# Kernel optimization log

Hardware: AMD Instinct MI355X
Metric: run time of the kernel (lower is better)

Reference implementation:

```python
import jax, jax.numpy as jnp
import numpy as np

B, T, P, N, U, L, K = 32, 12, 12, 512, 64, 2, 2
C = 2 * U  # combined_dim = input_dim(rnn_units) + rnn_units = 128


def setup_inputs():
    ks = jax.random.split(jax.random.key(0), 24)
    inp = {
        'x': jax.random.normal(ks[0], (B, T, N, 1), jnp.float32),
        'adj': jax.random.uniform(ks[1], (N, N), jnp.float32),
        'spatial_mask_1': 0.1 * jax.random.normal(ks[2], (N, N), jnp.float32),
        'spatial_mask_2': 0.1 * jax.random.normal(ks[3], (N, N), jnp.float32),
        'temporal_mask': 0.1 * jax.random.normal(ks[4], (T, N), jnp.float32),
        'fc_in_w': 0.1 * jax.random.normal(ks[5], (1, U), jnp.float32),
        'fc_in_b': jnp.zeros((U,), jnp.float32),
        'fc_out_w': 0.1 * jax.random.normal(ks[6], (U, 1), jnp.float32),
        'fc_out_b': jnp.zeros((1,), jnp.float32),
    }
    i = 7
    for pre in ('enc', 'dec'):
        for name, od in (('w_ru', 2 * U), ('w_c', U), ('w_ru2', 2 * U), ('w_c2', U)):
            inp[pre + '_' + name] = 0.08 * jax.random.normal(ks[i], (L, 2 * K, C, od), jnp.float32)
            i += 1
            inp[pre + '_' + name.replace('w', 'b')] = jnp.zeros((L, od), jnp.float32)
    return inp


def _supports(adj):
    # adj_hat = A + I; fwd = D_out^-1 A_hat ; bwd = D_in^-1 A_hat^T (inf -> 0)
    ah = adj + jnp.eye(adj.shape[0], dtype=adj.dtype)
    d_out = ah.sum(1)
    d_in = ah.sum(0)
    inv_out = jnp.where(d_out > 0, 1.0 / d_out, 0.0)
    inv_in = jnp.where(d_in > 0, 1.0 / d_in, 0.0)
    return inv_out[:, None] * ah, inv_in[:, None] * ah.T


def _dgc(x, sup, w, b):
    # x: [B,N,C]; sup: (fwd,bwd) each [N,N]; w: [2K,C,O]; b: [O]
    # The torch code expands x K times per support, so each k-slice of x_out is
    # identical: sum_k P_s @ w[k] == P_s @ w[sK:(s+1)K].sum(0). Same math, fused.
    pf = jnp.einsum('nm,bni->bmi', sup[0], x)
    pb = jnp.einsum('nm,bni->bmi', sup[1], x)
    return (jnp.einsum('bni,io->bno', pf, w[:K].sum(0))
            + jnp.einsum('bni,io->bno', pb, w[K:].sum(0)) + b)


def _cell(x, h, s1, s2, w_ru, b_ru, w_c, b_c, w_ru2, b_ru2, w_c2, b_c2):
    xh = jnp.concatenate([x, h], axis=-1)
    r1, u1 = jnp.split(jax.nn.sigmoid(_dgc(xh, s1, w_ru, b_ru)), 2, axis=-1)
    c1 = jnp.tanh(_dgc(jnp.concatenate([x, r1 * h], axis=-1), s1, w_c, b_c))
    r2, u2 = jnp.split(jax.nn.sigmoid(_dgc(xh, s2, w_ru2, b_ru2)), 2, axis=-1)
    c2 = jnp.tanh(_dgc(jnp.concatenate([x, r2 * h], axis=-1), s2, w_c2, b_c2))
    u = 0.5 * (u1 + u2)
    c = 0.5 * (c1 + c2)
    return (1.0 - u) * h + u * c


def _forward(x, adj, sm1, sm2, tm, fc_in_w, fc_in_b, fc_out_w, fc_out_b, enc, dec):
    x = x * (jnp.tanh(tm) + 1.0)[None, :, :, None]
    adj1 = adj * (jnp.tanh(0.5 * (sm1 + sm1.T)) + 1.0)
    adj2 = adj * (jnp.tanh(0.5 * (sm2 + sm2.T)) + 1.0)
    s1 = _supports(adj1)
    s2 = _supports(adj2)

    def run_layers(cells, inp, h):
        hs = []
        for i in range(L):
            hi = _cell(inp, h[i], s1, s2, *[p[i] for p in cells])
            hs.append(hi)
            inp = hi
        return jnp.stack(hs)

    def enc_step(h, xt):
        inp = xt @ fc_in_w + fc_in_b  # [B,N,U]
        return run_layers(enc, inp, h), None

    h0 = jnp.zeros((L, B, N, U), x.dtype)
    h, _ = jax.lax.scan(enc_step, h0, jnp.swapaxes(x, 0, 1))

    def dec_step(carry, _):
        h, go = carry
        inp = go @ fc_in_w + fc_in_b
        h = run_layers(dec, inp, h)
        out_t = h[-1] @ fc_out_w + fc_out_b  # [B,N,1]
        return (h, out_t), out_t

    _, outs = jax.lax.scan(dec_step, (h, jnp.zeros((B, N, 1), x.dtype)), None, length=P)
    return jnp.swapaxes(outs, 0, 1)[..., 0]  # [B,P,N]


def reference(x, adj, spatial_mask_1, spatial_mask_2, temporal_mask,
              fc_in_w, fc_in_b, fc_out_w, fc_out_b,
              enc_w_ru, enc_b_ru, enc_w_c, enc_b_c, enc_w_ru2, enc_b_ru2, enc_w_c2, enc_b_c2,
              dec_w_ru, dec_b_ru, dec_w_c, dec_b_c, dec_w_ru2, dec_b_ru2, dec_w_c2, dec_b_c2):
    enc = (enc_w_ru, enc_b_ru, enc_w_c, enc_b_c, enc_w_ru2, enc_b_ru2, enc_w_c2, enc_b_c2)
    dec = (dec_w_ru, dec_b_ru, dec_w_c, dec_b_c, dec_w_ru2, dec_b_ru2, dec_w_c2, dec_b_c2)
    return _forward(x, adj, spatial_mask_1, spatial_mask_2, temporal_mask,
                    fc_in_w, fc_in_b, fc_out_w, fc_out_b, enc, dec)
```

## Files before the change

kernel.cpp:

```cpp
#include <hip/hip_runtime.h>
#include <math.h>

#define NN 512
#define BB 32
#define UU 64
#define CC 128
#define TT 12
#define NP 12
#define RRR (NN*BB)

typedef _Float16 f16;
typedef f16 f16x8 __attribute__((ext_vector_type(8)));
typedef f16 f16x4 __attribute__((ext_vector_type(4)));
typedef float f32x4 __attribute__((ext_vector_type(4)));

__device__ __forceinline__ void gload16(const f16* g, f16* l) {
  __builtin_amdgcn_global_load_lds((const __attribute__((address_space(1))) void*)g,
                                   (__attribute__((address_space(3))) void*)l, 16, 0, 0);
}

static const size_t OFF_ST    = 0;
static const size_t OFF_AH    = OFF_ST   + (size_t)4*512*512;
static const size_t OFF_INVD  = OFF_AH   + (size_t)2*512*512;
static const size_t OFF_XH    = OFF_INVD + 2048;
static const size_t OFF_H     = OFF_XH   + (size_t)2*RRR*CC;
static const size_t OFF_RH    = OFF_H    + (size_t)2*RRR*UU;
static const size_t OFF_U     = OFF_RH   + (size_t)2*RRR*UU;
static const size_t OFF_SX    = OFF_U    + (size_t)2*RRR*UU;
static const size_t OFF_PS    = OFF_SX   + 16384;
static const size_t OFF_SROW  = OFF_PS   + 65536;
static const size_t OFF_F16   = OFF_SROW + 2048;
static const size_t OFF_ST16A = OFF_F16;
static const size_t OFF_ST16B = OFF_ST16A + 524288;
static const size_t OFF_XHT1  = OFF_ST16B + 524288;
static const size_t OFF_XHT2  = OFF_XHT1  + 1048576;
static const size_t OFF_RHT1  = OFF_XHT2  + 1048576;
static const size_t OFF_RHT2  = OFF_RHT1  + 1048576;
static const size_t OFF_P1    = OFF_RHT2  + 1048576;
static const size_t OFF_P2    = OFF_P1    + 4194304;
static const size_t OFF_Q1    = OFF_P2    + 4194304;
static const size_t OFF_Q2    = OFF_Q1    + 2097152;
static const size_t OFF_WT1   = OFF_Q2    + 2097152;
static const size_t OFF_WT2   = OFF_WT1   + 196608;

__global__ void k_build_ah(const float* __restrict__ adj, const float* __restrict__ sm1,
                           const float* __restrict__ sm2, float* __restrict__ ah) {
  int a = blockIdx.y, i = blockIdx.x;
  const float* sm = a ? sm2 : sm1;
  for (int j = threadIdx.x; j < NN; j += blockDim.x) {
    float m = tanhf(0.5f * (sm[i*NN + j] + sm[j*NN + i])) + 1.0f;
    ah[((size_t)a*NN + i)*NN + j] = adj[i*NN + j] * m + ((i == j) ? 1.0f : 0.0f);
  }
}

__global__ void k_deg(const float* __restrict__ ah, float* __restrict__ invd) {
  int a = blockIdx.y, n = blockIdx.x;
  const float* A = ah + (size_t)a*NN*NN;
  __shared__ float sr[256], sc[256];
  int t = threadIdx.x;
  sr[t] = A[(size_t)n*NN + t] + A[(size_t)n*NN + t + 256];
  sc[t] = A[(size_t)t*NN + n] + A[(size_t)(t+256)*NN + n];
  __syncthreads();
  for (int s = 128; s > 0; s >>= 1) {
    if (t < s) { sr[t] += sr[t+s]; sc[t] += sc[t+s]; }
    __syncthreads();
  }
  if (t == 0) {
    float dr = sr[0], dc = sc[0];
    invd[(a*2 + 0)*NN + n] = dr > 0.f ? 1.f/dr : 0.f;
    invd[(a*2 + 1)*NN + n] = dc > 0.f ? 1.f/dc : 0.f;
  }
}

__global__ void k_st(const float* __restrict__ ah, const float* __restrict__ invd,
                     float* __restrict__ ST) {
  int s = blockIdx.y, m = blockIdx.x;
  int a = s >> 1, dir = s & 1;
  const float* A = ah + (size_t)a*NN*NN;
  const float* inv = invd + (a*2 + dir)*NN;
  float* out = ST + ((size_t)s*NN + m)*NN;
  for (int n = threadIdx.x; n < NN; n += blockDim.x) {
    float v = dir ? A[(size_t)m*NN + n] : A[(size_t)n*NN + m];
    out[n] = inv[n] * v;
  }
}

__global__ void k_srow(const float* __restrict__ ST, float* __restrict__ SRow) {
  int row = blockIdx.x;
  int t = threadIdx.x;
  __shared__ float red[256];
  red[t] = ST[(size_t)row*512 + t] + ST[(size_t)row*512 + t + 256];
  __syncthreads();
  for (int s = 128; s > 0; s >>= 1) {
    if (t < s) red[t] += red[t+s];
    __syncthreads();
  }
  if (t == 0) SRow[row] = red[0];
}

__global__ void k_splitA(const float* __restrict__ s, f16* __restrict__ a1,
                         f16* __restrict__ a2, int total) {
  int i = blockIdx.x*blockDim.x + threadIdx.x;
  if (i >= total) return;
  float v = s[i] * 256.0f;
  f16 hi = (f16)v;
  a1[i] = hi;
  a2[i] = (f16)(v - (float)hi);
}

__global__ void k_wsumt(const float* __restrict__ w, f16* __restrict__ wt1,
                        f16* __restrict__ wt2, int O) {
  int idx = blockIdx.x*blockDim.x + threadIdx.x;
  int total = 2*2*O*128;
  if (idx >= total) return;
  int i  = idx & 127;
  int o  = (idx >> 7) % O;
  int fb = (idx / (128*O)) & 1;
  int l  = idx / (128*O*2);
  const float* wl = w + (((size_t)(l*4 + fb*2)*128 + i)*O + o);
  float v = (wl[0] + wl[(size_t)128*O]) * 256.0f;
  f16 hi = (f16)v;
  size_t dst = ((size_t)(l*2 + fb)*O + o)*128 + i;
  wt1[dst] = hi;
  wt2[dst] = (f16)(v - (float)hi);
}

__global__ void k_sx(const float* __restrict__ x, const float* __restrict__ tm,
                     float* __restrict__ SX, int t) {
  int R = blockIdx.x*blockDim.x + threadIdx.x;
  int b = R & 31, n = R >> 5;
  SX[R] = x[((size_t)b*TT + t)*NN + n] * (tanhf(tm[t*NN + n]) + 1.0f);
}

__launch_bounds__(256)
__global__ void k_ps(const float* __restrict__ ST, const float* __restrict__ SX,
                     float* __restrict__ PS) {
  int row = blockIdx.x;
  int t = threadIdx.x;
  int b = t & 31, g = t >> 5;
  const float* Sr = ST + (size_t)row*512 + g*64;
  const float* Sx = SX + (size_t)g*64*32 + b;
  float p = 0.f;
#pragma unroll
  for (int k = 0; k < 64; ++k) p = fmaf(Sr[k], Sx[(size_t)k*32], p);
  __shared__ float red[8][32];
  red[g][b] = p;
  __syncthreads();
  if (g == 0) {
    float s = 0.f;
#pragma unroll
    for (int q = 0; q < 8; ++q) s += red[q][b];
    PS[(size_t)row*32 + b] = s;
  }
}

__global__ void k_pxfill(const float* __restrict__ PS, const float* __restrict__ SRow,
                         const float* __restrict__ fiw, const float* __restrict__ fib,
                         f16* __restrict__ P1, f16* __restrict__ P2) {
  int idx = blockIdx.x*blockDim.x + threadIdx.x;
  int u8 = idx & 7;
  int R = (idx >> 3) & 16383;
  int sup = idx >> 17;
  int m = R >> 5, b = R & 31;
  float ps = PS[((size_t)sup*512 + m)*32 + b];
  float sr = SRow[(size_t)sup*512 + m];
  f16x8 h1, h2;
#pragma unroll
  for (int j = 0; j < 8; ++j) {
    int u = u8*8 + j;
    float v = ps*fiw[u] + sr*fib[u];
    f16 hi = (f16)v;
    h1[j] = hi;
    h2[j] = (f16)(v - (float)hi);
  }
  size_t dst = (size_t)sup*RRR*CC + (size_t)R*CC + u8*8;
  *(f16x8*)(P1 + dst) = h1;
  *(f16x8*)(P2 + dst) = h2;
}

__launch_bounds__(256)
__global__ void k_tsplit(const float* __restrict__ src, int lds_, long long srcZ,
                         f16* __restrict__ d1, f16* __restrict__ d2, long long dstZ) {
  __shared__ float tile[64][65];
  const float* S = src + (size_t)blockIdx.z*srcZ;
  f16* D1 = d1 + (size_t)blockIdx.z*dstZ;
  f16* D2 = d2 + (size_t)blockIdx.z*dstZ;
  int t = threadIdx.x;
  int c0 = blockIdx.x*64, k0 = blockIdx.y*64;
#pragma unroll
  for (int it = 0; it < 4; ++it) {
    int r = (t >> 4) + it*16;
    int c = (t & 15)*4;
    float4 v = *(const float4*)(S + (size_t)(k0 + r)*lds_ + c0 + c);
    tile[r][c] = v.x; tile[r][c+1] = v.y; tile[r][c+2] = v.z; tile[r][c+3] = v.w;
  }
  __syncthreads();
#pragma unroll
  for (int it = 0; it < 4; ++it) {
    int c = (t >> 4) + it*16;
    int ks = (t & 15)*4;
    f16x4 h1, h2;
#pragma unroll
    for (int j = 0; j < 4; ++j) {
      float v = tile[ks + j][c];
      f16 hi = (f16)v;
      h1[j] = hi;
      h2[j] = (f16)(v - (float)hi);
    }
    *(f16x4*)(D1 + (size_t)(c0 + c)*512 + k0 + ks) = h1;
    *(f16x4*)(D2 + (size_t)(c0 + c)*512 + k0 + ks) = h2;
  }
}

template<int MODE>
__launch_bounds__(256)
__global__ void k_mm16f(const f16* __restrict__ A1g, const f16* __restrict__ A2g, long long aZ,
                        const f16* __restrict__ B1g, const f16* __restrict__ B2g, long long bZ,
                        f16* __restrict__ C1g, f16* __restrict__ C2g, int ldc, long long cZ,
                        float scale) {
  const int bid = blockIdx.x;
  const int c = bid & 7, i = bid >> 3;
  int x, y; long long z;
  if (MODE == 0)      { x = 4*c + (i & 3); y = i >> 2; z = 0; }
  else if (MODE == 1) { z = c >> 2; x = 4*(c & 3) + (i & 3); y = i >> 2; }
  else                { x = 4*c + (i & 3); y = i >> 2; z = 0; }
  const f16* A1 = A1g + z*aZ; const f16* A2 = A2g + z*aZ;
  const f16* B1 = B1g + z*bZ; const f16* B2 = B2g + z*bZ;
  f16* C1 = C1g + z*cZ; f16* C2 = C2g + z*cZ;
  const int row0 = x*64, col0 = y*128;

  __shared__ __align__(16) f16 smem[24576];
  f16* As1 = smem;          f16* As2 = smem + 4096;
  f16* Bs1 = smem + 8192;   f16* Bs2 = smem + 16384;
  const int tid = threadIdx.x;
  const int lane = tid & 63, w = tid >> 6;
  const int rq = lane >> 3;
  const int gq = ((lane & 7) ^ rq) * 8;

  f32x4 acc[4][2];
#pragma unroll
  for (int m = 0; m < 4; ++m)
#pragma unroll
    for (int n = 0; n < 2; ++n) acc[m][n] = (f32x4){0.f,0.f,0.f,0.f};

  for (int k0 = 0; k0 < 512; k0 += 64) {
    __syncthreads();
#pragma unroll
    for (int q = 0; q < 2; ++q) {
      const int rloc = w*16 + q*8;
      gload16(A1 + (size_t)(row0 + rloc + rq)*512 + k0 + gq, As1 + rloc*64);
      gload16(A2 + (size_t)(row0 + rloc + rq)*512 + k0 + gq, As2 + rloc*64);
    }
#pragma unroll
    for (int q = 0; q < 4; ++q) {
      const int rloc = w*32 + q*8;
      gload16(B1 + (size_t)(col0 + rloc + rq)*512 + k0 + gq, Bs1 + rloc*64);
      gload16(B2 + (size_t)(col0 + rloc + rq)*512 + k0 + gq, Bs2 + rloc*64);
    }
    __syncthreads();
#pragma unroll
    for (int ks = 0; ks < 2; ++ks) {
      const int gk = ks*4 + (lane >> 4);
      f16x8 a1f[4], a2f[4], b1f[2], b2f[2];
#pragma unroll
      for (int m = 0; m < 4; ++m) {
        const int ra = m*16 + (lane & 15);
        const int sa = ra*64 + ((gk ^ (ra & 7))*8);
        a1f[m] = *(const f16x8*)(As1 + sa);
        a2f[m] = *(const f16x8*)(As2 + sa);
      }
#pragma unroll
      for (int n = 0; n < 2; ++n) {
        const int rb = w*32 + n*16 + (lane & 15);
        const int sb = rb*64 + ((gk ^ (rb & 7))*8);
        b1f[n] = *(const f16x8*)(Bs1 + sb);
        b2f[n] = *(const f16x8*)(Bs2 + sb);
      }
#pragma unroll
      for (int m = 0; m < 4; ++m)
#pragma unroll
        for (int n = 0; n < 2; ++n) {
          acc[m][n] = __builtin_amdgcn_mfma_f32_16x16x32_f16(a1f[m], b1f[n], acc[m][n], 0, 0, 0);
          acc[m][n] = __builtin_amdgcn_mfma_f32_16x16x32_f16(a1f[m], b2f[n], acc[m][n], 0, 0, 0);
          acc[m][n] = __builtin_amdgcn_mfma_f32_16x16x32_f16(a2f[m], b1f[n], acc[m][n], 0, 0, 0);
        }
    }
  }

  const int STR = 136;
  f16* cst = smem;
  __syncthreads();
#pragma unroll
  for (int pass = 0; pass < 2; ++pass) {
#pragma unroll
    for (int m = 0; m < 4; ++m)
#pragma unroll
      for (int n = 0; n < 2; ++n)
#pragma unroll
        for (int r = 0; r < 4; ++r) {
          const int rl = m*16 + (lane >> 4)*4 + r;
          const int cl = w*32 + n*16 + (lane & 15);
          float v = acc[m][n][r] * scale;
          f16 hi = (f16)v;
          cst[rl*STR + cl] = pass ? (f16)(v - (float)hi) : hi;
        }
    __syncthreads();
    f16* Cg = pass ? C2 : C1;
#pragma unroll
    for (int cI = 0; cI < 4; ++cI) {
      const int idx = cI*256 + tid;
      const int orow = idx >> 4, ocol = (idx & 15)*8;
      f16x8 v = *(const f16x8*)(cst + orow*STR + ocol);
      int gcol;
      if (MODE == 2) gcol = col0*2 + (ocol >> 6)*128 + 64 + (ocol & 63);
      else           gcol = col0 + ocol;
      *(f16x8*)(Cg + (size_t)(row0 + orow)*ldc + gcol) = v;
    }
    __syncthreads();
  }
}

__launch_bounds__(256)
__global__ void k_gatesmf(const f16* __restrict__ P1, const f16* __restrict__ P2,
                          const f16* __restrict__ W1g0, const f16* __restrict__ W2g0,
                          const f16* __restrict__ W1g1, const f16* __restrict__ W2g1,
                          const float* __restrict__ b0, const float* __restrict__ b1,
                          const float* __restrict__ h,
                          float* __restrict__ rh, float* __restrict__ ubuf) {
  const int g = blockIdx.z;
  const f16* W1 = g ? W1g1 : W1g0;
  const f16* W2 = g ? W2g1 : W2g0;
  const float* bias = g ? b1 : b0;
  float* rh_g = rh   + (size_t)g * RRR * UU;
  float* u_g  = ubuf + (size_t)g * RRR * UU;
  __shared__ __align__(16) f16 smem[24576];
  f16* As1 = smem;          f16* As2 = smem + 4096;
  f16* Bs1 = smem + 8192;   f16* Bs2 = smem + 16384;
  const int tid = threadIdx.x;
  const int lane = tid & 63, w = tid >> 6;
  const int R0 = blockIdx.x * 64;
  const int rq = lane >> 3;
  const int gq = ((lane & 7) ^ rq) * 8;

  f32x4 acc[4][2];
#pragma unroll
  for (int m = 0; m < 4; ++m)
#pragma unroll
    for (int n = 0; n < 2; ++n) acc[m][n] = (f32x4){0.f,0.f,0.f,0.f};

  for (int sup = 0; sup < 2; ++sup) {
    const f16* A1 = P1 + (size_t)(2*g + sup)*RRR*CC;
    const f16* A2 = P2 + (size_t)(2*g + sup)*RRR*CC;
    const f16* B1 = W1 + (size_t)sup*16384;
    const f16* B2 = W2 + (size_t)sup*16384;
    for (int k0 = 0; k0 < 128; k0 += 64) {
      __syncthreads();
#pragma unroll
      for (int q = 0; q < 1; ++q) {
        const int rloc = w*16 + q*8;
        gload16(A1 + (size_t)(R0 + rloc + rq)*128 + k0 + gq, As1 + rloc*64);
        gload16(A2 + (size_t)(R0 + rloc + rq)*128 + k0 + gq, As2 + rloc*64);
      }
#pragma unroll
      for (int q = 1; q < 2; ++q) {
        const int rloc = w*16 + q*8;
        gload16(A1 + (size_t)(R0 + rloc + rq)*128 + k0 + gq, As1 + rloc*64);
        gload16(A2 + (size_t)(R0 + rloc + rq)*128 + k0 + gq, As2 + rloc*64);
      }
#pragma unroll
      for (int q = 0; q < 4; ++q) {
        const int rloc = w*32 + q*8;
        gload16(B1 + (size_t)(rloc + rq)*128 + k0 + gq, Bs1 + rloc*64);
        gload16(B2 + (size_t)(rloc + rq)*128 + k0 + gq, Bs2 + rloc*64);
      }
      __syncthreads();
#pragma unroll
      for (int ks = 0; ks < 2; ++ks) {
        const int gk = ks*4 + (lane >> 4);
        f16x8 a1f[4], a2f[4], b1f[2], b2f[2];
#pragma unroll
        for (int m = 0; m < 4; ++m) {
          const int ra = m*16 + (lane & 15);
          const int sa = ra*64 + ((gk ^ (ra & 7))*8);
          a1f[m] = *(const f16x8*)(As1 + sa);
          a2f[m] = *(const f16x8*)(As2 + sa);
        }
#pragma unroll
        for (int n = 0; n < 2; ++n) {
          const int rb = w*32 + n*16 + (lane & 15);
          const int sb = rb*64 + ((gk ^ (rb & 7))*8);
          b1f[n] = *(const f16x8*)(Bs1 + sb);
          b2f[n] = *(const f16x8*)(Bs2 + sb);
        }
#pragma unroll
        for (int m = 0; m < 4; ++m)
#pragma unroll
          for (int n = 0; n < 2; ++n) {
            acc[m][n] = __builtin_amdgcn_mfma_f32_16x16x32_f16(a1f[m], b1f[n], acc[m][n], 0, 0, 0);
            acc[m][n] = __builtin_amdgcn_mfma_f32_16x16x32_f16(a1f[m], b2f[n], acc[m][n], 0, 0, 0);
            acc[m][n] = __builtin_amdgcn_mfma_f32_16x16x32_f16(a2f[m], b1f[n], acc[m][n], 0, 0, 0);
          }
      }
    }
  }
#pragma unroll
  for (int m = 0; m < 4; ++m) {
    const int row = R0 + m*16 + (lane >> 4)*4;
#pragma unroll
    for (int n = 0; n < 2; ++n) {
      const int o = w*32 + n*16 + (lane & 15);
#pragma unroll
      for (int r = 0; r < 4; ++r) {
        const int R = row + r;
        float v = acc[m][n][r] * 0.00390625f + bias[o];
        float sg = 1.f / (1.f + expf(-v));
        if (o < 64) rh_g[(size_t)R*UU + o] = sg * h[(size_t)R*UU + o];
        else        u_g[(size_t)R*UU + o - 64] = sg;
      }
    }
  }
}

__launch_bounds__(256)
__global__ void k_candupd(const f16* __restrict__ P1, const f16* __restrict__ P2,
                          const f16* __restrict__ Q1, const f16* __restrict__ Q2,
                          const f16* __restrict__ Wc1g0, const f16* __restrict__ Wc2g0,
                          const f16* __restrict__ Wc1g1, const f16* __restrict__ Wc2g1,
                          const float* __restrict__ b0, const float* __restrict__ b1,
                          const float* __restrict__ ubuf,
                          float* __restrict__ h, float* __restrict__ xh_self,
                          float* __restrict__ xh_next) {
  __shared__ __align__(16) f16 smem[12288];
  f16* As1 = smem;          f16* As2 = smem + 2048;
  f16* Bs1 = smem + 4096;   f16* Bs2 = smem + 8192;
  const int tid = threadIdx.x;
  const int lane = tid & 63, w = tid >> 6;
  const int R0 = blockIdx.x * 32;
  const int rq = lane >> 3;
  const int gq = ((lane & 7) ^ rq) * 8;
  const int wm = w & 1, wn = w >> 1;

  f32x4 acc[2][2];
#pragma unroll
  for (int g = 0; g < 2; ++g)
#pragma unroll
    for (int n = 0; n < 2; ++n) acc[g][n] = (f32x4){0.f,0.f,0.f,0.f};

#pragma unroll
  for (int g = 0; g < 2; ++g) {
    const f16* W1 = g ? Wc1g1 : Wc1g0;
    const f16* W2 = g ? Wc2g1 : Wc2g0;
#pragma unroll
    for (int seg = 0; seg < 4; ++seg) {
      const int sup = seg >> 1, isQ = seg & 1;
      const f16* A1 = isQ ? (Q1 + ((size_t)g*2 + sup)*1048576)
                          : (P1 + (size_t)(2*g + sup)*RRR*CC);
      const f16* A2 = isQ ? (Q2 + ((size_t)g*2 + sup)*1048576)
                          : (P2 + (size_t)(2*g + sup)*RRR*CC);
      const int lda = isQ ? 64 : 128;
      const f16* B1 = W1 + (size_t)sup*8192 + (isQ ? 64 : 0);
      const f16* B2 = W2 + (size_t)sup*8192 + (isQ ? 64 : 0);
      __syncthreads();
      {
        const int rloc = w*8;
        gload16(A1 + (size_t)(R0 + rloc + rq)*lda + gq, As1 + rloc*64);
        gload16(A2 + (size_t)(R0 + rloc + rq)*lda + gq, As2 + rloc*64);
      }
#pragma unroll
      for (int q = 0; q < 2; ++q) {
        const int rloc = w*16 + q*8;
        gload16(B1 + (size_t)(rloc + rq)*128 + gq, Bs1 + rloc*64);
        gload16(B2 + (size_t)(rloc + rq)*128 + gq, Bs2 + rloc*64);
      }
      __syncthreads();
#pragma unroll
      for (int ks = 0; ks < 2; ++ks) {
        const int gk = ks*4 + (lane >> 4);
        const int ra = wm*16 + (lane & 15);
        const int sa = ra*64 + ((gk ^ (ra & 7))*8);
        f16x8 a1f = *(const f16x8*)(As1 + sa);
        f16x8 a2f = *(const f16x8*)(As2 + sa);
        f16x8 b1f[2], b2f[2];
#pragma unroll
        for (int n = 0; n < 2; ++n) {
          const int rb = wn*32 + n*16 + (lane & 15);
          const int sb = rb*64 + ((gk ^ (rb & 7))*8);
          b1f[n] = *(const f16x8*)(Bs1 + sb);
          b2f[n] = *(const f16x8*)(Bs2 + sb);
        }
#pragma unroll
        for (int n = 0; n < 2; ++n) {
          acc[g][n] = __builtin_amdgcn_mfma_f32_16x16x32_f16(a1f, b1f[n], acc[g][n], 0, 0, 0);
          acc[g][n] = __builtin_amdgcn_mfma_f32_16x16x32_f16(a1f, b2f[n], acc[g][n], 0, 0, 0);
          acc[g][n] = __builtin_amdgcn_mfma_f32_16x16x32_f16(a2f, b1f[n], acc[g][n], 0, 0, 0);
        }
      }
    }
  }
#pragma unroll
  for (int n = 0; n < 2; ++n) {
    const int o = wn*32 + n*16 + (lane & 15);
#pragma unroll
    for (int r = 0; r < 4; ++r) {
      const int R = R0 + wm*16 + (lane >> 4)*4 + r;
      const size_t idx = (size_t)R*UU + o;
      float c1 = tanhf(acc[0][n][r] * 0.00390625f + b0[o]);
      float c2 = tanhf(acc[1][n][r] * 0.00390625f + b1[o]);
      float u = 0.5f*(ubuf[idx] + ubuf[(size_t)RRR*UU + idx]);
      float cc = 0.5f*(c1 + c2);
      float hn = (1.f - u)*h[idx] + u*cc;
      h[idx] = hn;
      if (xh_self) xh_self[(size_t)R*CC + 64 + o] = hn;
      if (xh_next) xh_next[(size_t)R*CC + o] = hn;
    }
  }
}

__global__ void k_out(const float* __restrict__ h1, const float* __restrict__ fow,
                      const float* __restrict__ fob, float* __restrict__ out,
                      float* __restrict__ SX, int p) {
  int R = blockIdx.x*blockDim.x + threadIdx.x;
  int b = R & 31, n = R >> 5;
  const float* hr = h1 + (size_t)R*UU;
  float s = fob[0];
#pragma unroll
  for (int u = 0; u < UU; ++u) s = fmaf(hr[u], fow[u], s);
  out[(size_t)b*(NP*NN) + (size_t)p*NN + n] = s;
  SX[R] = s;
}

extern "C" void kernel_launch(void* const* d_in, const int* in_sizes, int n_in,
                              void* d_out, int out_size, void* d_ws, size_t ws_size,
                              hipStream_t stream) {
  (void)in_sizes; (void)n_in; (void)out_size; (void)ws_size;
  const float* x   = (const float*)d_in[0];
  const float* adj = (const float*)d_in[1];
  const float* sm1 = (const float*)d_in[2];
  const float* sm2 = (const float*)d_in[3];
  const float* tm  = (const float*)d_in[4];
  const float* fiw = (const float*)d_in[5];
  const float* fib = (const float*)d_in[6];
  const float* fow = (const float*)d_in[7];
  const float* fob = (const float*)d_in[8];

  float* WS   = (float*)d_ws;
  float* ST   = WS + OFF_ST;
  float* AH   = WS + OFF_AH;
  float* INVD = WS + OFF_INVD;
  float* XH   = WS + OFF_XH;
  float* H    = WS + OFF_H;
  float* RH   = WS + OFF_RH;
  float* Ubuf = WS + OFF_U;
  float* SX   = WS + OFF_SX;
  float* PS   = WS + OFF_PS;
  float* SRow = WS + OFF_SROW;
  f16* ST1  = (f16*)(WS + OFF_ST16A);
  f16* ST2  = (f16*)(WS + OFF_ST16B);
  f16* XHT1 = (f16*)(WS + OFF_XHT1);
  f16* XHT2 = (f16*)(WS + OFF_XHT2);
  f16* RHT1 = (f16*)(WS + OFF_RHT1);
  f16* RHT2 = (f16*)(WS + OFF_RHT2);
  f16* P1   = (f16*)(WS + OFF_P1);
  f16* P2   = (f16*)(WS + OFF_P2);
  f16* Q1   = (f16*)(WS + OFF_Q1);
  f16* Q2   = (f16*)(WS + OFF_Q2);
  f16* WT1  = (f16*)(WS + OFF_WT1);
  f16* WT2  = (f16*)(WS + OFF_WT2);

  k_build_ah<<<dim3(512,2),256,0,stream>>>(adj, sm1, sm2, AH);
  k_deg<<<dim3(512,2),256,0,stream>>>(AH, INVD);
  k_st<<<dim3(512,4),256,0,stream>>>(AH, INVD, ST);
  k_splitA<<<4096,256,0,stream>>>(ST, ST1, ST2, 2048*512);
  k_srow<<<2048,256,0,stream>>>(ST, SRow);

  const int widx[8] = {9, 11, 13, 15, 17, 19, 21, 23};
  const int Osz[8]  = {128, 64, 128, 64, 128, 64, 128, 64};
  const size_t woff16[8] = {0, 65536, 98304, 163840, 196608, 262144, 294912, 360448};
  for (int tau = 0; tau < 8; ++tau) {
    int total = 2*2*Osz[tau]*128;
    k_wsumt<<<(total + 255)/256, 256, 0, stream>>>((const float*)d_in[widx[tau]],
                                                   WT1 + woff16[tau], WT2 + woff16[tau],
                                                   Osz[tau]);
  }

  hipMemsetAsync(XH, 0, (size_t)2*RRR*CC*sizeof(float), stream);
  hipMemsetAsync(H,  0, (size_t)2*RRR*UU*sizeof(float), stream);

  const float inv256 = 1.0f/256.0f;

  for (int step = 0; step < TT + NP; ++step) {
    const bool enc = step < TT;
    const int ph = enc ? 0 : 1;
    if (enc)             k_sx<<<64,256,0,stream>>>(x, tm, SX, step);
    else if (step == TT) hipMemsetAsync(SX, 0, 16384*sizeof(float), stream);

    k_ps<<<2048,256,0,stream>>>(ST, SX, PS);

    for (int l = 0; l < 2; ++l) {
      float* xh1  = XH + (size_t)RRR*CC;
      float* h_l  = H  + (size_t)l*RRR*UU;
      const size_t lru = (size_t)l*2*128*128;
      const size_t lc  = (size_t)l*2*64*128;
      const f16* Wru1a = WT1 + woff16[ph*4+0] + lru;
      const f16* Wru2a = WT2 + woff16[ph*4+0] + lru;
      const f16* Wru1b = WT1 + woff16[ph*4+2] + lru;
      const f16* Wru2b = WT2 + woff16[ph*4+2] + lru;
      const f16* Wc1a  = WT1 + woff16[ph*4+1] + lc;
      const f16* Wc2a  = WT2 + woff16[ph*4+1] + lc;
      const f16* Wc1b  = WT1 + woff16[ph*4+3] + lc;
      const f16* Wc2b  = WT2 + woff16[ph*4+3] + lc;
      const float* bru  = (const float*)d_in[enc?10:18] + (size_t)l*128;
      const float* bc   = (const float*)d_in[enc?12:20] + (size_t)l*64;
      const float* bru2 = (const float*)d_in[enc?14:22] + (size_t)l*128;
      const float* bc2  = (const float*)d_in[enc?16:24] + (size_t)l*64;

      if (l == 0) {
        k_tsplit<<<dim3(32,8,1),256,0,stream>>>(h_l, 2048, 0, XHT1, XHT2, 0);
        k_mm16f<2><<<512,256,0,stream>>>(ST1, ST2, 0, XHT1, XHT2, 0,
                                         P1, P2, 4096, 0, inv256);
        k_pxfill<<<2048,256,0,stream>>>(PS, SRow, fiw, fib, P1, P2);
      } else {
        k_tsplit<<<dim3(64,8,1),256,0,stream>>>(xh1, 4096, 0, XHT1, XHT2, 0);
        k_mm16f<0><<<1024,256,0,stream>>>(ST1, ST2, 0, XHT1, XHT2, 0,
                                          P1, P2, 4096, 0, inv256);
      }
      k_gatesmf<<<dim3(256,1,2),256,0,stream>>>(P1, P2, Wru1a, Wru2a, Wru1b, Wru2b,
                                                bru, bru2, h_l, RH, Ubuf);
      k_tsplit<<<dim3(32,8,2),256,0,stream>>>(RH, 2048, (long long)RRR*UU,
                                              RHT1, RHT2, (long long)2048*512);
      k_mm16f<1><<<512,256,0,stream>>>(ST1, ST2, (long long)1024*512,
                                       RHT1, RHT2, (long long)2048*512,
                                       Q1, Q2, 2048, (long long)1024*2048, inv256);
      k_candupd<<<512,256,0,stream>>>(P1, P2, Q1, Q2, Wc1a, Wc2a, Wc1b, Wc2b,
                                      bc, bc2, Ubuf, h_l,
                                      (l == 1) ? xh1 : nullptr,
                                      (l == 0) ? xh1 : nullptr);
    }
    if (!enc) {
      int p = step - TT;
      k_out<<<64,256,0,stream>>>(H + (size_t)RRR*UU, fow, fob,
                                 (float*)d_out, SX, p);
    }
  }
}
```

Baseline: 4.473 ms.

## Fuse support-times-input reduction into P fill and halve gate tile rows

The k_ps reduction is merged with k_pxfill into one kernel, k_psfill, which computes the per-row support-times-x sums in shared memory and writes the f16 split P entries straight away. This drops one launch per step and the PS round trip through global memory. Separately, k_gatesmf now uses 32-row tiles instead of 64, doubling its grid to 1024 blocks for better CU occupancy. The cost is more redundant reloading of the weight tiles and fewer MFMAs per LDS load.

```diff
diff --git a/kernel.cpp b/kernel.cpp
--- a/kernel.cpp
+++ b/kernel.cpp
@@ -133,8 +133,10 @@
 }
 
 __launch_bounds__(256)
-__global__ void k_ps(const float* __restrict__ ST, const float* __restrict__ SX,
-                     float* __restrict__ PS) {
+__global__ void k_psfill(const float* __restrict__ ST, const float* __restrict__ SX,
+                         const float* __restrict__ SRow,
+                         const float* __restrict__ fiw, const float* __restrict__ fib,
+                         f16* __restrict__ P1, f16* __restrict__ P2) {
   int row = blockIdx.x;
   int t = threadIdx.x;
   int b = t & 31, g = t >> 5;
@@ -144,36 +146,30 @@
 #pragma unroll
   for (int k = 0; k < 64; ++k) p = fmaf(Sr[k], Sx[(size_t)k*32], p);
   __shared__ float red[8][32];
+  __shared__ float ps[32];
   red[g][b] = p;
   __syncthreads();
-  if (g == 0) {
+  if (t < 32) {
     float s = 0.f;
 #pragma unroll
-    for (int q = 0; q < 8; ++q) s += red[q][b];
-    PS[(size_t)row*32 + b] = s;
-  }
-}
-
-__global__ void k_pxfill(const float* __restrict__ PS, const float* __restrict__ SRow,
-                         const float* __restrict__ fiw, const float* __restrict__ fib,
-                         f16* __restrict__ P1, f16* __restrict__ P2) {
-  int idx = blockIdx.x*blockDim.x + threadIdx.x;
-  int u8 = idx & 7;
-  int R = (idx >> 3) & 16383;
-  int sup = idx >> 17;
-  int m = R >> 5, b = R & 31;
-  float ps = PS[((size_t)sup*512 + m)*32 + b];
-  float sr = SRow[(size_t)sup*512 + m];
+    for (int q = 0; q < 8; ++q) s += red[q][t];
+    ps[t] = s;
+  }
+  __syncthreads();
+  const float sr = SRow[row];
+  const int sup = row >> 9, m = row & 511;
+  const int b2 = t >> 3, u8 = t & 7;
+  const float psv = ps[b2];
   f16x8 h1, h2;
 #pragma unroll
   for (int j = 0; j < 8; ++j) {
     int u = u8*8 + j;
-    float v = ps*fiw[u] + sr*fib[u];
+    float v = psv*fiw[u] + sr*fib[u];
     f16 hi = (f16)v;
     h1[j] = hi;
     h2[j] = (f16)(v - (float)hi);
   }
-  size_t dst = (size_t)sup*RRR*CC + (size_t)R*CC + u8*8;
+  size_t dst = (size_t)sup*RRR*CC + (size_t)(m*32 + b2)*CC + u8*8;
   *(f16x8*)(P1 + dst) = h1;
   *(f16x8*)(P2 + dst) = h2;
 }
@@ -333,18 +329,18 @@
   const float* bias = g ? b1 : b0;
   float* rh_g = rh   + (size_t)g * RRR * UU;
   float* u_g  = ubuf + (size_t)g * RRR * UU;
-  __shared__ __align__(16) f16 smem[24576];
-  f16* As1 = smem;          f16* As2 = smem + 4096;
-  f16* Bs1 = smem + 8192;   f16* Bs2 = smem + 16384;
+  __shared__ __align__(16) f16 smem[20480];
+  f16* As1 = smem;          f16* As2 = smem + 2048;
+  f16* Bs1 = smem + 4096;   f16* Bs2 = smem + 12288;
   const int tid = threadIdx.x;
   const int lane = tid & 63, w = tid >> 6;
-  const int R0 = blockIdx.x * 64;
+  const int R0 = blockIdx.x * 32;
   const int rq = lane >> 3;
   const int gq = ((lane & 7) ^ rq) * 8;
 
-  f32x4 acc[4][2];
-#pragma unroll
-  for (int m = 0; m < 4; ++m)
+  f32x4 acc[2][2];
+#pragma unroll
+  for (int m = 0; m < 2; ++m)
 #pragma unroll
     for (int n = 0; n < 2; ++n) acc[m][n] = (f32x4){0.f,0.f,0.f,0.f};
 
@@ -355,15 +351,8 @@
     const f16* B2 = W2 + (size_t)sup*16384;
     for (int k0 = 0; k0 < 128; k0 += 64) {
       __syncthreads();
-#pragma unroll
-      for (int q = 0; q < 1; ++q) {
-        const int rloc = w*16 + q*8;
-        gload16(A1 + (size_t)(R0 + rloc + rq)*128 + k0 + gq, As1 + rloc*64);
-        gload16(A2 + (size_t)(R0 + rloc + rq)*128 + k0 + gq, As2 + rloc*64);
-      }
-#pragma unroll
-      for (int q = 1; q < 2; ++q) {
-        const int rloc = w*16 + q*8;
+      {
+        const int rloc = w*8;
         gload16(A1 + (size_t)(R0 + rloc + rq)*128 + k0 + gq, As1 + rloc*64);
         gload16(A2 + (size_t)(R0 + rloc + rq)*128 + k0 + gq, As2 + rloc*64);
       }
@@ -377,9 +366,9 @@
 #pragma unroll
       for (int ks = 0; ks < 2; ++ks) {
         const int gk = ks*4 + (lane >> 4);
-        f16x8 a1f[4], a2f[4], b1f[2], b2f[2];
-#pragma unroll
-        for (int m = 0; m < 4; ++m) {
+        f16x8 a1f[2], a2f[2], b1f[2], b2f[2];
+#pragma unroll
+        for (int m = 0; m < 2; ++m) {
           const int ra = m*16 + (lane & 15);
           const int sa = ra*64 + ((gk ^ (ra & 7))*8);
           a1f[m] = *(const f16x8*)(As1 + sa);
@@ -393,7 +382,7 @@
           b2f[n] = *(const f16x8*)(Bs2 + sb);
         }
 #pragma unroll
-        for (int m = 0; m < 4; ++m)
+        for (int m = 0; m < 2; ++m)
 #pragma unroll
           for (int n = 0; n < 2; ++n) {
             acc[m][n] = __builtin_amdgcn_mfma_f32_16x16x32_f16(a1f[m], b1f[n], acc[m][n], 0, 0, 0);
@@ -404,7 +393,7 @@
     }
   }
 #pragma unroll
-  for (int m = 0; m < 4; ++m) {
+  for (int m = 0; m < 2; ++m) {
     const int row = R0 + m*16 + (lane >> 4)*4;
 #pragma unroll
     for (int n = 0; n < 2; ++n) {
@@ -552,7 +541,6 @@
   float* RH   = WS + OFF_RH;
   float* Ubuf = WS + OFF_U;
   float* SX   = WS + OFF_SX;
-  float* PS   = WS + OFF_PS;
   float* SRow = WS + OFF_SROW;
   f16* ST1  = (f16*)(WS + OFF_ST16A);
   f16* ST2  = (f16*)(WS + OFF_ST16B);
@@ -593,8 +581,6 @@
     const int ph = enc ? 0 : 1;
     if (enc)             k_sx<<<64,256,0,stream>>>(x, tm, SX, step);
     else if (step == TT) hipMemsetAsync(SX, 0, 16384*sizeof(float), stream);
-
-    k_ps<<<2048,256,0,stream>>>(ST, SX, PS);
 
     for (int l = 0; l < 2; ++l) {
       float* xh1  = XH + (size_t)RRR*CC;
@@ -618,13 +604,13 @@
         k_tsplit<<<dim3(32,8,1),256,0,stream>>>(h_l, 2048, 0, XHT1, XHT2, 0);
         k_mm16f<2><<<512,256,0,stream>>>(ST1, ST2, 0, XHT1, XHT2, 0,
                                          P1, P2, 4096, 0, inv256);
-        k_pxfill<<<2048,256,0,stream>>>(PS, SRow, fiw, fib, P1, P2);
+        k_psfill<<<2048,256,0,stream>>>(ST, SX, SRow, fiw, fib, P1, P2);
       } else {
         k_tsplit<<<dim3(64,8,1),256,0,stream>>>(xh1, 4096, 0, XHT1, XHT2, 0);
         k_mm16f<0><<<1024,256,0,stream>>>(ST1, ST2, 0, XHT1, XHT2, 0,
                                           P1, P2, 4096, 0, inv256);
       }
-      k_gatesmf<<<dim3(256,1,2),256,0,stream>>>(P1, P2, Wru1a, Wru2a, Wru1b, Wru2b,
+      k_gatesmf<<<dim3(512,1,2),256,0,stream>>>(P1, P2, Wru1a, Wru2a, Wru1b, Wru2b,
                                                 bru, bru2, h_l, RH, Ubuf);
       k_tsplit<<<dim3(32,8,2),256,0,stream>>>(RH, 2048, (long long)RRR*UU,
                                               RHT1, RHT2, (long long)2048*512);
```

Result: faster. 4.301 ms, median of 2 (-3.8%).
